# Kernel tuning notes

Hardware: AMD Instinct MI355X
Metric: run time of the kernel (lower is better)

Reference implementation:

```python
import jax, jax.numpy as jnp
import numpy as np

N_NODES = 50000
N_EDGES = 800000
D_IN = 128
D_HID = 128
D_OUT = 1
N_GRAPHS = 64


def gcn_conv(x, edge_index, W, b):
    """PyG GCNConv: add self-loops, symmetric deg^-1/2 normalization, xW, scatter-add, +bias."""
    n = x.shape[0]
    loops = jnp.arange(n, dtype=edge_index.dtype)
    row = jnp.concatenate([edge_index[0], loops])  # source nodes
    col = jnp.concatenate([edge_index[1], loops])  # destination nodes
    deg = jax.ops.segment_sum(jnp.ones_like(col, dtype=x.dtype), col, num_segments=n)
    dinv = jax.lax.rsqrt(jnp.maximum(deg, 1.0))  # deg >= 1 due to self-loops
    norm = dinv[row] * dinv[col]                 # [E+N]
    h = x @ W                                    # [N, d_out] dense GEMM first (cheaper than per-edge)
    msgs = h[row] * norm[:, None]                # gather + scale, [E+N, d_out]
    out = jax.ops.segment_sum(msgs, col, num_segments=n)  # scatter-add
    return out + b


def setup_inputs() -> dict:
    key = jax.random.key(0)
    ks = jax.random.split(key, 12)
    x = jax.random.normal(ks[0], (N_NODES, D_IN), dtype=jnp.float32)
    edge_index = jax.random.randint(ks[1], (2, N_EDGES), 0, N_NODES, dtype=jnp.int64)
    batch = jnp.sort(jax.random.randint(ks[2], (N_NODES,), 0, N_GRAPHS, dtype=jnp.int64))
    s_in = 1.0 / np.sqrt(D_IN)
    s_hid = 1.0 / np.sqrt(D_HID)
    W0 = jax.random.uniform(ks[3], (D_IN, D_HID), jnp.float32, -s_in, s_in)
    b0 = jnp.zeros((D_HID,), jnp.float32)
    W1 = jax.random.uniform(ks[4], (D_HID, D_HID), jnp.float32, -s_hid, s_hid)
    b1 = jnp.zeros((D_HID,), jnp.float32)
    W2 = jax.random.uniform(ks[5], (D_HID, D_HID), jnp.float32, -s_hid, s_hid)
    b2 = jnp.zeros((D_HID,), jnp.float32)
    fc_w = jax.random.uniform(ks[6], (D_HID, D_OUT), jnp.float32, -s_hid, s_hid)
    fc_b = jax.random.uniform(ks[7], (D_OUT,), jnp.float32, -s_hid, s_hid)
    return {"x": x, "edge_index": edge_index, "batch": batch,
            "W0": W0, "b0": b0, "W1": W1, "b1": b1, "W2": W2, "b2": b2,
            "fc_w": fc_w, "fc_b": fc_b}


def reference(x, edge_index, batch, W0, b0, W1, b1, W2, b2, fc_w, fc_b):
    h = x
    for W, b in ((W0, b0), (W1, b1), (W2, b2)):  # 3 GCN layers (structural, not data loop)
        h = jax.nn.relu(gcn_conv(h, edge_index, W, b))
    # global_mean_pool over graph ids
    sums = jax.ops.segment_sum(h, batch, num_segments=N_GRAPHS)          # [G, d]
    counts = jax.ops.segment_sum(jnp.ones((h.shape[0],), h.dtype), batch, num_segments=N_GRAPHS)
    pooled = sums / jnp.maximum(counts, 1.0)[:, None]
    return pooled @ fc_w + fc_b  # [G, 1]
```

## Files before the change

### kernel.cpp

```cpp
#include <hip/hip_runtime.h>

#define DH 128
#define NGRAPH 64

static __device__ __forceinline__ float4 f4fma(float a, float4 b, float4 c) {
  c.x = fmaf(a, b.x, c.x); c.y = fmaf(a, b.y, c.y);
  c.z = fmaf(a, b.z, c.z); c.w = fmaf(a, b.w, c.w);
  return c;
}

__global__ void init_deg_k(int* __restrict__ deg, int n) {
  int i = blockIdx.x * blockDim.x + threadIdx.x;
  if (i < n) deg[i] = 1;
}

__global__ void count_deg_k(const int* __restrict__ col, int* __restrict__ deg, int e) {
  int i = blockIdx.x * blockDim.x + threadIdx.x;
  if (i < e) atomicAdd(&deg[col[i]], 1);
}

__global__ void dinv_k(const int* __restrict__ deg, float* __restrict__ dinv, int n) {
  int i = blockIdx.x * blockDim.x + threadIdx.x;
  if (i < n) dinv[i] = rsqrtf((float)deg[i]);
}

__global__ __launch_bounds__(512) void scan1_k(const int* __restrict__ deg, int* __restrict__ incl,
                                               int* __restrict__ blksum, int n) {
  __shared__ int s[512];
  int t = threadIdx.x;
  int i = blockIdx.x * 512 + t;
  int v = (i < n) ? (deg[i] - 1) : 0;
  s[t] = v;
  __syncthreads();
  #pragma unroll
  for (int off = 1; off < 512; off <<= 1) {
    int x = (t >= off) ? s[t - off] : 0;
    __syncthreads();
    s[t] += x;
    __syncthreads();
  }
  if (i < n) incl[i] = s[t];
  if (t == 511) blksum[blockIdx.x] = s[511];
}

__global__ __launch_bounds__(128) void scan2_k(int* __restrict__ blksum, int nb) {
  __shared__ int s[128];
  int t = threadIdx.x;
  int v = (t < nb) ? blksum[t] : 0;
  s[t] = v;
  __syncthreads();
  #pragma unroll
  for (int off = 1; off < 128; off <<= 1) {
    int x = (t >= off) ? s[t - off] : 0;
    __syncthreads();
    s[t] += x;
    __syncthreads();
  }
  if (t < nb) blksum[t] = s[t] - v;
}

__global__ __launch_bounds__(512) void scan3_k(const int* __restrict__ deg, int* __restrict__ ptr,
                                               const int* __restrict__ blkoff, int* __restrict__ cursor,
                                               int n, int e) {
  int i = blockIdx.x * 512 + threadIdx.x;
  if (i < n) {
    int cnt = deg[i] - 1;
    int excl = ptr[i] - cnt + blkoff[i >> 9];
    ptr[i] = excl;
    cursor[i] = excl;
  }
  if (i == 0) ptr[n] = e;
}

__global__ void scatter_k(const int* __restrict__ row, const int* __restrict__ col,
                          int* __restrict__ cursor, int* __restrict__ csr_src, int e) {
  int i = blockIdx.x * blockDim.x + threadIdx.x;
  if (i < e) {
    int c = col[i];
    int pos = atomicAdd(&cursor[c], 1);
    csr_src[pos] = row[i];
  }
}

__global__ __launch_bounds__(256, 3) void gemm_k(const float* __restrict__ A, const float* __restrict__ W,
                                                 float* __restrict__ C, int M) {
  __shared__ float xs[64][64];
  __shared__ float ws[64][128];
  const int tid = threadIdx.x;
  const int tx = tid & 31;
  const int ty = tid >> 5;
  const int m_base = blockIdx.x * 64;

  float4 acc[8];
  #pragma unroll
  for (int i = 0; i < 8; i++) acc[i] = make_float4(0.f, 0.f, 0.f, 0.f);

  for (int kc = 0; kc < 128; kc += 64) {
    const float4* Wg = (const float4*)(W + kc * DH);
    float4* wsv = (float4*)ws;
    #pragma unroll
    for (int i = 0; i < 8; i++) wsv[tid + 256 * i] = Wg[tid + 256 * i];
    #pragma unroll
    for (int i = 0; i < 4; i++) {
      int f = tid + 256 * i;
      int m = f >> 4;
      int k4 = (f & 15) << 2;
      int r = m_base + m;
      if (r >= M) r = M - 1;
      *(float4*)&xs[m][k4] = *(const float4*)(A + (size_t)r * DH + kc + k4);
    }
    __syncthreads();
    #pragma unroll 4
    for (int k = 0; k < 64; k += 4) {
      float4 wb0 = *(const float4*)&ws[k + 0][tx * 4];
      float4 wb1 = *(const float4*)&ws[k + 1][tx * 4];
      float4 wb2 = *(const float4*)&ws[k + 2][tx * 4];
      float4 wb3 = *(const float4*)&ws[k + 3][tx * 4];
      #pragma unroll
      for (int i = 0; i < 8; i++) {
        float4 xa = *(const float4*)&xs[ty * 8 + i][k];
        acc[i] = f4fma(xa.x, wb0, acc[i]);
        acc[i] = f4fma(xa.y, wb1, acc[i]);
        acc[i] = f4fma(xa.z, wb2, acc[i]);
        acc[i] = f4fma(xa.w, wb3, acc[i]);
      }
    }
    __syncthreads();
  }
  float* Cp = C + (size_t)(m_base + ty * 8) * DH + tx * 4;
  #pragma unroll
  for (int i = 0; i < 8; i++) *(float4*)(Cp + (size_t)i * DH) = acc[i];
}

__global__ __launch_bounds__(256) void aggregate_k(const float* __restrict__ hW, const float* __restrict__ dinv,
                                                   const int* __restrict__ ptr, const int* __restrict__ csr_src,
                                                   const float* __restrict__ bias, float* __restrict__ out, int n) {
  int wave = threadIdx.x >> 6;
  int lane = threadIdx.x & 63;
  int node = blockIdx.x * 4 + wave;
  if (node >= n) return;
  const float2* h2 = (const float2*)hW;
  float di = dinv[node];
  float2 acc = h2[(size_t)node * 64 + lane];
  acc.x *= di * di; acc.y *= di * di;
  int e0 = ptr[node], e1 = ptr[node + 1];
  for (int e = e0; e < e1; ++e) {
    int s = csr_src[e];
    float w = dinv[s] * di;
    float2 hv = h2[(size_t)s * 64 + lane];
    acc.x = fmaf(hv.x, w, acc.x);
    acc.y = fmaf(hv.y, w, acc.y);
  }
  float2 b = *(const float2*)(bias + lane * 2);
  acc.x = fmaxf(acc.x + b.x, 0.f);
  acc.y = fmaxf(acc.y + b.y, 0.f);
  ((float2*)out)[(size_t)node * 64 + lane] = acc;
}

__global__ void count_batch_k(const int* __restrict__ batch, int* __restrict__ gcnt, int n) {
  int i = blockIdx.x * blockDim.x + threadIdx.x;
  bool active = (i < n);
  int g = active ? batch[i] : 0;
  unsigned long long act = __ballot(active);
  if (!active) return;
  int first = __ffsll((long long)act) - 1;
  int g0 = __shfl(g, first);
  bool uni = __all(g == g0);
  int lane = threadIdx.x & 63;
  if (uni) {
    if (lane == first) atomicAdd(&gcnt[g], (int)__popcll(act));
  } else {
    atomicAdd(&gcnt[g], 1);
  }
}

#define POOL_CHUNK 50
__global__ __launch_bounds__(128) void pool_partial_k(const float* __restrict__ h, const int* __restrict__ batch,
                                                      float* __restrict__ pooled, int n) {
  int n0 = blockIdx.x * POOL_CHUNK;
  if (n0 >= n) return;
  int n1 = n0 + POOL_CHUNK; if (n1 > n) n1 = n;
  int d = threadIdx.x;
  float acc = 0.f;
  int gp = batch[n0];
  for (int i = n0; i < n1; ++i) {
    int g = batch[i];
    if (g != gp) { atomicAdd(&pooled[(size_t)gp * DH + d], acc); acc = 0.f; gp = g; }
    acc += h[(size_t)i * DH + d];
  }
  atomicAdd(&pooled[(size_t)gp * DH + d], acc);
}

__global__ void final_k(const float* __restrict__ pooled, const int* __restrict__ gcnt,
                        const float* __restrict__ fcw, const float* __restrict__ fcb,
                        float* __restrict__ out) {
  int g = threadIdx.x;
  if (g >= NGRAPH) return;
  float c = fmaxf((float)gcnt[g], 1.f);
  float s = 0.f;
  #pragma unroll 4
  for (int d = 0; d < DH; ++d) s = fmaf(pooled[(size_t)g * DH + d] / c, fcw[d], s);
  out[g] = s + fcb[0];
}

extern "C" void kernel_launch(void* const* d_in, const int* in_sizes, int n_in,
                              void* d_out, int out_size, void* d_ws, size_t ws_size,
                              hipStream_t stream) {
  const float* x    = (const float*)d_in[0];
  const int*   ei   = (const int*)d_in[1];
  const int*   batch= (const int*)d_in[2];
  const float* W0   = (const float*)d_in[3];
  const float* b0   = (const float*)d_in[4];
  const float* W1   = (const float*)d_in[5];
  const float* b1   = (const float*)d_in[6];
  const float* W2   = (const float*)d_in[7];
  const float* b2   = (const float*)d_in[8];
  const float* fcw  = (const float*)d_in[9];
  const float* fcb  = (const float*)d_in[10];
  float* out = (float*)d_out;

  const int N = in_sizes[0] / DH;
  const int E = in_sizes[1] / 2;
  const int* row = ei;
  const int* col = ei + E;
  const int MPAD = ((N + 63) / 64) * 64;

  char* ws = (char*)d_ws;
  size_t off = 0;
  auto carve = [&](size_t bytes) -> char* {
    char* p = ws + off;
    off = (off + bytes + 255) & ~(size_t)255;
    return p;
  };
  float* bufA    = (float*)carve((size_t)MPAD * DH * 4);
  float* bufB    = (float*)carve((size_t)MPAD * DH * 4);
  int*   deg     = (int*)carve((size_t)N * 4);
  float* dinv    = (float*)carve((size_t)N * 4);
  int*   csr_ptr = (int*)carve((size_t)(N + 1) * 4);
  int*   cursor  = (int*)carve((size_t)N * 4);
  int*   csr_src = (int*)carve((size_t)E * 4);
  int*   blksum  = (int*)carve(128 * 4);
  int*   gcnt    = (int*)carve(NGRAPH * 4);
  float* pooled  = (float*)carve((size_t)NGRAPH * DH * 4);
  (void)ws_size; (void)n_in; (void)out_size;

  const int nb256N = (N + 255) / 256;
  const int nb256E = (E + 255) / 256;
  const int nbScan = (N + 511) / 512;

  hipMemsetAsync(gcnt, 0, NGRAPH * 4, stream);
  hipMemsetAsync(pooled, 0, (size_t)NGRAPH * DH * 4, stream);

  init_deg_k<<<nb256N, 256, 0, stream>>>(deg, N);
  count_deg_k<<<nb256E, 256, 0, stream>>>(col, deg, E);
  count_batch_k<<<nb256N, 256, 0, stream>>>(batch, gcnt, N);
  dinv_k<<<nb256N, 256, 0, stream>>>(deg, dinv, N);

  scan1_k<<<nbScan, 512, 0, stream>>>(deg, csr_ptr, blksum, N);
  scan2_k<<<1, 128, 0, stream>>>(blksum, nbScan);
  scan3_k<<<nbScan, 512, 0, stream>>>(deg, csr_ptr, blksum, cursor, N, E);
  scatter_k<<<nb256E, 256, 0, stream>>>(row, col, cursor, csr_src, E);

  const int gemmBlocks = MPAD / 64;
  const int aggBlocks = (N + 3) / 4;

  gemm_k<<<gemmBlocks, 256, 0, stream>>>(x, W0, bufA, N);
  aggregate_k<<<aggBlocks, 256, 0, stream>>>(bufA, dinv, csr_ptr, csr_src, b0, bufB, N);
  gemm_k<<<gemmBlocks, 256, 0, stream>>>(bufB, W1, bufA, N);
  aggregate_k<<<aggBlocks, 256, 0, stream>>>(bufA, dinv, csr_ptr, csr_src, b1, bufB, N);
  gemm_k<<<gemmBlocks, 256, 0, stream>>>(bufB, W2, bufA, N);
  aggregate_k<<<aggBlocks, 256, 0, stream>>>(bufA, dinv, csr_ptr, csr_src, b2, bufB, N);

  const int poolBlocks = (N + POOL_CHUNK - 1) / POOL_CHUNK;
  pool_partial_k<<<poolBlocks, 128, 0, stream>>>(bufB, batch, pooled, N);
  final_k<<<1, 64, 0, stream>>>(pooled, gcnt, fcw, fcb, out);
}
```

Before: 586.1 us.

## Pre-scale GEMM rows by dinv and unroll neighbor aggregation with multiple accumulators

Factors the symmetric normalization so the GEMM epilogue multiplies each output row by dinv[src], and aggregation becomes a plain sum of pre-scaled rows, multiplied once by dinv[dst]. This removes the per-edge dinv gather and multiply. The aggregation loop is unrolled by four with independent accumulators to keep more gathers in flight. Degree init and the dinv kernel are folded into a memset and the scan3 kernel, cutting launches. The change alters the floating-point summation order.

```diff
diff --git a/kernel.cpp b/kernel.cpp
--- a/kernel.cpp
+++ b/kernel.cpp
@@ -9,19 +9,9 @@
   return c;
 }
 
-__global__ void init_deg_k(int* __restrict__ deg, int n) {
-  int i = blockIdx.x * blockDim.x + threadIdx.x;
-  if (i < n) deg[i] = 1;
-}
-
 __global__ void count_deg_k(const int* __restrict__ col, int* __restrict__ deg, int e) {
   int i = blockIdx.x * blockDim.x + threadIdx.x;
   if (i < e) atomicAdd(&deg[col[i]], 1);
-}
-
-__global__ void dinv_k(const int* __restrict__ deg, float* __restrict__ dinv, int n) {
-  int i = blockIdx.x * blockDim.x + threadIdx.x;
-  if (i < n) dinv[i] = rsqrtf((float)deg[i]);
 }
 
 __global__ __launch_bounds__(512) void scan1_k(const int* __restrict__ deg, int* __restrict__ incl,
@@ -29,7 +19,7 @@
   __shared__ int s[512];
   int t = threadIdx.x;
   int i = blockIdx.x * 512 + t;
-  int v = (i < n) ? (deg[i] - 1) : 0;
+  int v = (i < n) ? deg[i] : 0;
   s[t] = v;
   __syncthreads();
   #pragma unroll
@@ -61,13 +51,14 @@
 
 __global__ __launch_bounds__(512) void scan3_k(const int* __restrict__ deg, int* __restrict__ ptr,
                                                const int* __restrict__ blkoff, int* __restrict__ cursor,
-                                               int n, int e) {
+                                               float* __restrict__ dinv, int n, int e) {
   int i = blockIdx.x * 512 + threadIdx.x;
   if (i < n) {
-    int cnt = deg[i] - 1;
+    int cnt = deg[i];
     int excl = ptr[i] - cnt + blkoff[i >> 9];
     ptr[i] = excl;
     cursor[i] = excl;
+    dinv[i] = rsqrtf((float)(cnt + 1));
   }
   if (i == 0) ptr[n] = e;
 }
@@ -83,6 +74,7 @@
 }
 
 __global__ __launch_bounds__(256, 3) void gemm_k(const float* __restrict__ A, const float* __restrict__ W,
+                                                 const float* __restrict__ dinv,
                                                  float* __restrict__ C, int M) {
   __shared__ float xs[64][64];
   __shared__ float ws[64][128];
@@ -127,34 +119,56 @@
     }
     __syncthreads();
   }
-  float* Cp = C + (size_t)(m_base + ty * 8) * DH + tx * 4;
-  #pragma unroll
-  for (int i = 0; i < 8; i++) *(float4*)(Cp + (size_t)i * DH) = acc[i];
-}
-
-__global__ __launch_bounds__(256) void aggregate_k(const float* __restrict__ hW, const float* __restrict__ dinv,
+  #pragma unroll
+  for (int i = 0; i < 8; i++) {
+    int r = m_base + ty * 8 + i;
+    int rc = (r < M) ? r : (M - 1);
+    float dsc = dinv[rc];
+    acc[i].x *= dsc; acc[i].y *= dsc; acc[i].z *= dsc; acc[i].w *= dsc;
+    *(float4*)(C + (size_t)r * DH + tx * 4) = acc[i];
+  }
+}
+
+__global__ __launch_bounds__(256) void aggregate_k(const float* __restrict__ hs, const float* __restrict__ dinv,
                                                    const int* __restrict__ ptr, const int* __restrict__ csr_src,
                                                    const float* __restrict__ bias, float* __restrict__ out, int n) {
   int wave = threadIdx.x >> 6;
   int lane = threadIdx.x & 63;
   int node = blockIdx.x * 4 + wave;
   if (node >= n) return;
-  const float2* h2 = (const float2*)hW;
+  const float2* h2 = (const float2*)hs;
   float di = dinv[node];
-  float2 acc = h2[(size_t)node * 64 + lane];
-  acc.x *= di * di; acc.y *= di * di;
   int e0 = ptr[node], e1 = ptr[node + 1];
-  for (int e = e0; e < e1; ++e) {
+  float2 a0 = h2[(size_t)node * 64 + lane];
+  float2 a1 = make_float2(0.f, 0.f);
+  float2 a2 = make_float2(0.f, 0.f);
+  float2 a3 = make_float2(0.f, 0.f);
+  int e = e0;
+  for (; e + 4 <= e1; e += 4) {
+    int s0 = csr_src[e + 0];
+    int s1 = csr_src[e + 1];
+    int s2 = csr_src[e + 2];
+    int s3 = csr_src[e + 3];
+    float2 v0 = h2[(size_t)s0 * 64 + lane];
+    float2 v1 = h2[(size_t)s1 * 64 + lane];
+    float2 v2 = h2[(size_t)s2 * 64 + lane];
+    float2 v3 = h2[(size_t)s3 * 64 + lane];
+    a0.x += v0.x; a0.y += v0.y;
+    a1.x += v1.x; a1.y += v1.y;
+    a2.x += v2.x; a2.y += v2.y;
+    a3.x += v3.x; a3.y += v3.y;
+  }
+  for (; e < e1; ++e) {
     int s = csr_src[e];
-    float w = dinv[s] * di;
-    float2 hv = h2[(size_t)s * 64 + lane];
-    acc.x = fmaf(hv.x, w, acc.x);
-    acc.y = fmaf(hv.y, w, acc.y);
-  }
+    float2 v = h2[(size_t)s * 64 + lane];
+    a0.x += v.x; a0.y += v.y;
+  }
+  float sx = (a0.x + a1.x) + (a2.x + a3.x);
+  float sy = (a0.y + a1.y) + (a2.y + a3.y);
   float2 b = *(const float2*)(bias + lane * 2);
-  acc.x = fmaxf(acc.x + b.x, 0.f);
-  acc.y = fmaxf(acc.y + b.y, 0.f);
-  ((float2*)out)[(size_t)node * 64 + lane] = acc;
+  sx = fmaxf(fmaf(sx, di, b.x), 0.f);
+  sy = fmaxf(fmaf(sy, di, b.y), 0.f);
+  ((float2*)out)[(size_t)node * 64 + lane] = make_float2(sx, sy);
 }
 
 __global__ void count_batch_k(const int* __restrict__ batch, int* __restrict__ gcnt, int n) {
@@ -248,27 +262,26 @@
   const int nb256E = (E + 255) / 256;
   const int nbScan = (N + 511) / 512;
 
+  hipMemsetAsync(deg, 0, (size_t)N * 4, stream);
   hipMemsetAsync(gcnt, 0, NGRAPH * 4, stream);
   hipMemsetAsync(pooled, 0, (size_t)NGRAPH * DH * 4, stream);
 
-  init_deg_k<<<nb256N, 256, 0, stream>>>(deg, N);
   count_deg_k<<<nb256E, 256, 0, stream>>>(col, deg, E);
   count_batch_k<<<nb256N, 256, 0, stream>>>(batch, gcnt, N);
-  dinv_k<<<nb256N, 256, 0, stream>>>(deg, dinv, N);
 
   scan1_k<<<nbScan, 512, 0, stream>>>(deg, csr_ptr, blksum, N);
   scan2_k<<<1, 128, 0, stream>>>(blksum, nbScan);
-  scan3_k<<<nbScan, 512, 0, stream>>>(deg, csr_ptr, blksum, cursor, N, E);
+  scan3_k<<<nbScan, 512, 0, stream>>>(deg, csr_ptr, blksum, cursor, dinv, N, E);
   scatter_k<<<nb256E, 256, 0, stream>>>(row, col, cursor, csr_src, E);
 
   const int gemmBlocks = MPAD / 64;
   const int aggBlocks = (N + 3) / 4;
 
-  gemm_k<<<gemmBlocks, 256, 0, stream>>>(x, W0, bufA, N);
+  gemm_k<<<gemmBlocks, 256, 0, stream>>>(x, W0, dinv, bufA, N);
   aggregate_k<<<aggBlocks, 256, 0, stream>>>(bufA, dinv, csr_ptr, csr_src, b0, bufB, N);
-  gemm_k<<<gemmBlocks, 256, 0, stream>>>(bufB, W1, bufA, N);
+  gemm_k<<<gemmBlocks, 256, 0, stream>>>(bufB, W1, dinv, bufA, N);
   aggregate_k<<<aggBlocks, 256, 0, stream>>>(bufA, dinv, csr_ptr, csr_src, b1, bufB, N);
-  gemm_k<<<gemmBlocks, 256, 0, stream>>>(bufB, W2, bufA, N);
+  gemm_k<<<gemmBlocks, 256, 0, stream>>>(bufB, W2, dinv, bufA, N);
   aggregate_k<<<aggBlocks, 256, 0, stream>>>(bufA, dinv, csr_ptr, csr_src, b2, bufB, N);
 
   const int poolBlocks = (N + POOL_CHUNK - 1) / POOL_CHUNK;
```

After: 502.8 us. 14.2% less time.
